# Optimization experiments

Measured on AMD Instinct MI355X. Metric: run time of the kernel, lower is better.

Reference implementation:

```python
import jax, jax.numpy as jnp
import numpy as np
import math

H = 8
D_MODEL = 512
D_K = D_MODEL // H          # 64, per-head value dim
D_QK = D_K // 2             # 32, per-head query/key dim
B, S = 2, 4096


def setup_inputs() -> dict:
    key = jax.random.key(0)
    ks = jax.random.split(key, 20)
    std = 0.02
    inp = {
        'query': jax.random.normal(ks[0], (B, S, D_MODEL), jnp.float32),
        'key':   jax.random.normal(ks[1], (B, S, D_MODEL), jnp.float32),
        'value': jax.random.normal(ks[2], (B, S, D_MODEL), jnp.float32),
        # MLP_q: d_model -> 2*d_model -> d_model/2
        'Wq1': jax.random.normal(ks[3], (D_MODEL, 2 * D_MODEL), jnp.float32) * std,
        'bq1': jnp.zeros((2 * D_MODEL,), jnp.float32),
        'Wq2': jax.random.normal(ks[4], (2 * D_MODEL, D_MODEL // 2), jnp.float32) * std,
        'bq2': jnp.zeros((D_MODEL // 2,), jnp.float32),
        # MLP_k: d_model -> 2*d_model -> d_model/2
        'Wk1': jax.random.normal(ks[5], (D_MODEL, 2 * D_MODEL), jnp.float32) * std,
        'bk1': jnp.zeros((2 * D_MODEL,), jnp.float32),
        'Wk2': jax.random.normal(ks[6], (2 * D_MODEL, D_MODEL // 2), jnp.float32) * std,
        'bk2': jnp.zeros((D_MODEL // 2,), jnp.float32),
        # linear_v and output linear: d_model -> d_model
        'Wv': jax.random.normal(ks[7], (D_MODEL, D_MODEL), jnp.float32) * std,
        'bv': jnp.zeros((D_MODEL,), jnp.float32),
        'Wo': jax.random.normal(ks[8], (D_MODEL, D_MODEL), jnp.float32) * std,
        'bo': jnp.zeros((D_MODEL,), jnp.float32),
    }
    return inp


def reference(query, key, value, Wq1, bq1, Wq2, bq2, Wk1, bk1, Wk2, bk2, Wv, bv, Wo, bo):
    nb = query.shape[0]
    # MLP_q / MLP_k: Linear -> exact GELU -> Linear (torch GELU default is erf)
    q = jax.nn.gelu(query @ Wq1 + bq1, approximate=False) @ Wq2 + bq2   # [B,S,D_MODEL/2]
    k = jax.nn.gelu(key   @ Wk1 + bk1, approximate=False) @ Wk2 + bk2   # [B,S,D_MODEL/2]
    v = value @ Wv + bv                                                  # [B,S,D_MODEL]

    q = q.reshape(nb, -1, H, D_QK)   # [B,S,H,d_qk]
    k = k.reshape(nb, -1, H, D_QK)
    v = v.reshape(nb, -1, H, D_K)    # [B,S,H,d_k]

    # scores scaled by sqrt(d_qk) since query.size(-1) == d_k//2 in the original
    scores = jnp.einsum('bqhd,bkhd->bhqk', q, k) / math.sqrt(D_QK)  # [B,H,S,S]
    p = jax.nn.softmax(scores, axis=-1)
    x = jnp.einsum('bhqk,bkhd->bqhd', p, v).reshape(nb, -1, H * D_K)  # [B,S,D_MODEL]
    return x @ Wo + bo
```

## Files before the change

### kernel.cpp

```cpp
#include <hip/hip_runtime.h>
#include <math.h>

typedef __attribute__((ext_vector_type(8))) short short8;
typedef __bf16 bf16x8 __attribute__((ext_vector_type(8)));
typedef __attribute__((ext_vector_type(4))) float f32x4;
typedef __attribute__((ext_vector_type(16))) float f32x16;

__device__ inline short f2bf(float f) {
    unsigned u = __builtin_bit_cast(unsigned, f);
    u += 0x7fff + ((u >> 16) & 1);
    return (short)(u >> 16);
}
__device__ inline float bf2f(short h) {
    return __builtin_bit_cast(float, ((unsigned)(unsigned short)h) << 16);
}
__device__ inline float gelu_f(float x) {
    return 0.5f * x * (1.f + erff(x * 0.70710678118654752f));
}

__global__ __launch_bounds__(256) void cast3(
    const float* __restrict__ q, const float* __restrict__ k,
    const float* __restrict__ v,
    short* __restrict__ qc, short* __restrict__ kc, short* __restrict__ vc)
{
    const float* src = blockIdx.y == 0 ? q : (blockIdx.y == 1 ? k : v);
    short* dst = blockIdx.y == 0 ? qc : (blockIdx.y == 1 ? kc : vc);
    size_t i = ((size_t)blockIdx.x * 256 + threadIdx.x) * 8;
    float4 a = *(const float4*)(src + i);
    float4 b = *(const float4*)(src + i + 4);
    short8 o;
    o[0] = f2bf(a.x); o[1] = f2bf(a.y); o[2] = f2bf(a.z); o[3] = f2bf(a.w);
    o[4] = f2bf(b.x); o[5] = f2bf(b.y); o[6] = f2bf(b.z); o[7] = f2bf(b.w);
    *(short8*)(void*)(dst + i) = o;
}

__global__ __launch_bounds__(256) void wprep(
    const float* __restrict__ Wq1, const float* __restrict__ Wk1,
    const float* __restrict__ Wq2, const float* __restrict__ Wk2,
    const float* __restrict__ Wv,  const float* __restrict__ Wo,
    short* __restrict__ Wq1t, short* __restrict__ Wk1t,
    short* __restrict__ Wq2t, short* __restrict__ Wk2t,
    short* __restrict__ Wvt,  short* __restrict__ Wo3t)
{
    int id = blockIdx.x;
    const float* W; short* Wt; int K, N; int t3 = 0;
    if (id < 512)       { W = Wq1; Wt = Wq1t; K = 512;  N = 1024; }
    else if (id < 1024) { W = Wk1; Wt = Wk1t; K = 512;  N = 1024; id -= 512; }
    else if (id < 1280) { W = Wq2; Wt = Wq2t; K = 1024; N = 256;  id -= 1024; }
    else if (id < 1536) { W = Wk2; Wt = Wk2t; K = 1024; N = 256;  id -= 1280; }
    else if (id < 1792) { W = Wv;  Wt = Wvt;  K = 512;  N = 512;  id -= 1536; }
    else                { W = Wo;  Wt = Wo3t; K = 512;  N = 512;  id -= 1792; t3 = 1; }
    int nx = N >> 5;
    int n0 = (id % nx) * 32, k0 = (id / nx) * 32;

    __shared__ float T[32][33];
    int tid = threadIdx.x;
    int r = tid >> 3, c4 = (tid & 7) * 4;
    float4 v = *(const float4*)&W[(size_t)(k0 + r) * N + n0 + c4];
    T[r][c4 + 0] = v.x; T[r][c4 + 1] = v.y; T[r][c4 + 2] = v.z; T[r][c4 + 3] = v.w;
    __syncthreads();
    if (!t3) {
        short4 o;
        o.x = f2bf(T[c4 + 0][r]);
        o.y = f2bf(T[c4 + 1][r]);
        o.z = f2bf(T[c4 + 2][r]);
        o.w = f2bf(T[c4 + 3][r]);
        *(short4*)&Wt[(size_t)(n0 + r) * K + k0 + c4] = o;
    } else {
        short4 hi, lo;
        float f;
        f = T[c4 + 0][r]; hi.x = f2bf(f); lo.x = f2bf(f - bf2f(hi.x));
        f = T[c4 + 1][r]; hi.y = f2bf(f); lo.y = f2bf(f - bf2f(hi.y));
        f = T[c4 + 2][r]; hi.z = f2bf(f); lo.z = f2bf(f - bf2f(hi.z));
        f = T[c4 + 3][r]; hi.w = f2bf(f); lo.w = f2bf(f - bf2f(hi.w));
        short* d = Wt + (size_t)(n0 + r) * 3 * K + k0 + c4;
        *(short4*)d = hi;
        *(short4*)(d + K) = lo;
        *(short4*)(d + 2 * K) = hi;
    }
}

template <int ACT, int OUTF32, int BN>
__global__ __launch_bounds__(256) void gemm_bt(
    const short* __restrict__ A0, const short* __restrict__ A1,
    const short* __restrict__ B0, const short* __restrict__ B1,
    const float* __restrict__ b0, const float* __restrict__ b1,
    void* C0_, void* C1_,
    float s0, float s1, int nbn, int N, int K)
{
    constexpr int NT = BN / 32;
    const int z = blockIdx.z;
    const short* A = z ? A1 : A0;
    const short* B = z ? B1 : B0;
    const float* bias = z ? b1 : b0;
    void* C_ = z ? C1_ : C0_;
    const float scale = z ? s1 : s0;

    const int L = blockIdx.x;
    const int xcd = L & 7;
    const int per = L >> 3;
    const int bn = (per % nbn) * BN;
    const int bm = ((per / nbn) * 8 + xcd) * 128;

    const int tid = threadIdx.x;
    const int w = tid >> 6;
    const int lane = tid & 63;
    const int l15 = lane & 15, quad = lane >> 4;
    const int wm = (w >> 1) * 64, wn = (w & 1) * (BN / 2);

    __shared__ __align__(16) short As[128 * 64];
    __shared__ __align__(16) short Bs[BN * 64];

    f32x4 acc[4][NT];
#pragma unroll
    for (int mt = 0; mt < 4; ++mt)
#pragma unroll
        for (int nt = 0; nt < NT; ++nt) acc[mt][nt] = (f32x4){0.f, 0.f, 0.f, 0.f};

    for (int k0 = 0; k0 < K; k0 += 64) {
#pragma unroll
        for (int i = 0; i < 4; ++i) {
            int ga = tid + i * 256;
            int row = ga >> 3, g = ga & 7;
            short8 aval = *(const short8*)(const void*)&A[(size_t)(bm + row) * K + k0 + g * 8];
            *(short8*)(void*)&As[row * 64 + ((g ^ (row & 7)) * 8)] = aval;
        }
#pragma unroll
        for (int i = 0; i < BN / 32; ++i) {
            int gb = tid + i * 256;
            int row = gb >> 3, g = gb & 7;
            short8 bval = *(const short8*)(const void*)&B[(size_t)(bn + row) * K + k0 + g * 8];
            *(short8*)(void*)&Bs[row * 64 + ((g ^ (row & 7)) * 8)] = bval;
        }
        __syncthreads();

#pragma unroll
        for (int ks = 0; ks < 2; ++ks) {
            bf16x8 af[4], bfr[NT];
#pragma unroll
            for (int t = 0; t < 4; ++t) {
                int row = wm + t * 16 + l15;
                af[t] = __builtin_bit_cast(bf16x8,
                    *(const short8*)(const void*)&As[row * 64 + (((ks * 4 + quad) ^ (row & 7)) * 8)]);
            }
#pragma unroll
            for (int t = 0; t < NT; ++t) {
                int row = wn + t * 16 + l15;
                bfr[t] = __builtin_bit_cast(bf16x8,
                    *(const short8*)(const void*)&Bs[row * 64 + (((ks * 4 + quad) ^ (row & 7)) * 8)]);
            }
#pragma unroll
            for (int mt = 0; mt < 4; ++mt)
#pragma unroll
                for (int nt = 0; nt < NT; ++nt)
                    acc[mt][nt] = __builtin_amdgcn_mfma_f32_16x16x32_bf16(af[mt], bfr[nt], acc[mt][nt], 0, 0, 0);
        }
        __syncthreads();
    }

    float bv[NT];
#pragma unroll
    for (int nt = 0; nt < NT; ++nt) bv[nt] = bias[bn + wn + nt * 16 + l15];
#pragma unroll
    for (int mt = 0; mt < 4; ++mt)
#pragma unroll
        for (int r = 0; r < 4; ++r) {
            int row = bm + wm + mt * 16 + quad * 4 + r;
#pragma unroll
            for (int nt = 0; nt < NT; ++nt) {
                float v = acc[mt][nt][r] + bv[nt];
                if (ACT) v = gelu_f(v);
                v *= scale;
                int col = bn + wn + nt * 16 + l15;
                if (OUTF32) ((float*)C_)[(size_t)row * N + col] = v;
                else        ((short*)C_)[(size_t)row * N + col] = f2bf(v);
            }
        }
}

__global__ __launch_bounds__(256) void repack_k(
    const short* __restrict__ kb, short* __restrict__ kfr)
{
    const int kt = blockIdx.x, bh = blockIdx.y;
    const int b = bh >> 3, h = bh & 7;
    const int t = threadIdx.x;
    const int c = t >> 6, l = t & 63;
    const int nt = c >> 1, ks = c & 1;
    int key = kt * 64 + nt * 32 + (l & 31);
    int k = ks * 16 + (l >> 5) * 8;
    short8 v = *(const short8*)(const void*)&kb[(size_t)(b * 4096 + key) * 256 + h * 32 + k];
    *(short8*)(void*)&kfr[((((size_t)bh * 64 + kt) * 4 + c) * 64 + l) * 8] = v;
}

__global__ __launch_bounds__(256) void repack_v(
    const short* __restrict__ vbb, short* __restrict__ vfr)
{
    const int kt = blockIdx.x, bh = blockIdx.y;
    const int b = bh >> 3, h = bh & 7;
    const int t = threadIdx.x;
    __shared__ short Vt[64][72];

#pragma unroll
    for (int it = 0; it < 2; ++it) {
        int idx = t + it * 256;
        int keyr = idx >> 3, c8 = (idx & 7) * 8;
        *(short8*)(void*)&Vt[keyr][c8] =
            *(const short8*)(const void*)&vbb[(size_t)(b * 4096 + kt * 64 + keyr) * 512 + h * 64 + c8];
    }
    __syncthreads();
#pragma unroll
    for (int it = 0; it < 2; ++it) {
        int chunk = (t >> 6) * 2 + it;
        int l = t & 63;
        int dt = chunk >> 2, ks = chunk & 3;
        short8 o;
#pragma unroll
        for (int j = 0; j < 8; ++j)
            o[j] = Vt[ks * 16 + (l >> 5) * 8 + j][dt * 32 + (l & 31)];
        *(short8*)(void*)&vfr[((((size_t)bh * 64 + kt) * 8 + chunk) * 64 + l) * 8] = o;
    }
}

__global__ __launch_bounds__(256) void flash_ks(
    const short* __restrict__ qb, const short* __restrict__ kfr,
    const short* __restrict__ vfr, short* __restrict__ xb3)
{
    const int L = blockIdx.x;
    const int xcd = L & 7;
    const int idx = L >> 3;
    const int bh = xcd * 2 + (idx & 1);
    const int qt = idx >> 1;
    const int b = bh >> 3, h = bh & 7;
    const int w = threadIdx.x >> 6;
    const int qg = w >> 1;
    const int kh = w & 1;
    const int lane = threadIdx.x & 63;
    const int l31 = lane & 31;
    const int half = lane >> 5;

    __shared__ __align__(16) char smem[18432];
    short* Pw = (short*)smem + w * 2304;

    const short* qrow = qb + (size_t)(b * 4096 + qt * 64 + qg * 32 + l31) * 256 + h * 32 + half * 8;
    bf16x8 qf0 = __builtin_bit_cast(bf16x8, *(const short8*)(const void*)qrow);
    bf16x8 qf1 = __builtin_bit_cast(bf16x8, *(const short8*)(const void*)(qrow + 16));

    f32x16 O0{}, O1{};
    float la = 0.f;

    const short* kbase = kfr + ((size_t)bh * 64) * 4 * 512 + lane * 8;
    const short* vbase = vfr + ((size_t)bh * 64) * 8 * 512 + lane * 8;

#pragma unroll 1
    for (int t = 0; t < 32; ++t) {
        const int kt = kh * 32 + t;
        bf16x8 kc[4], vc[8];
        const short* kp = kbase + (size_t)kt * 4 * 512;
        const short* vp = vbase + (size_t)kt * 8 * 512;
#pragma unroll
        for (int c = 0; c < 4; ++c)
            kc[c] = __builtin_bit_cast(bf16x8, *(const short8*)(const void*)(kp + c * 512));
#pragma unroll
        for (int c = 0; c < 8; ++c)
            vc[c] = __builtin_bit_cast(bf16x8, *(const short8*)(const void*)(vp + c * 512));

        f32x16 zero{};
        f32x16 s0 = __builtin_amdgcn_mfma_f32_32x32x16_bf16(kc[0], qf0, zero, 0, 0, 0);
        s0 = __builtin_amdgcn_mfma_f32_32x32x16_bf16(kc[1], qf1, s0, 0, 0, 0);
        f32x16 s1 = __builtin_amdgcn_mfma_f32_32x32x16_bf16(kc[2], qf0, zero, 0, 0, 0);
        s1 = __builtin_amdgcn_mfma_f32_32x32x16_bf16(kc[3], qf1, s1, 0, 0, 0);

#pragma unroll
        for (int nt = 0; nt < 2; ++nt) {
            const f32x16& s = nt ? s1 : s0;
#pragma unroll
            for (int r2 = 0; r2 < 4; ++r2) {
                float p0 = __builtin_amdgcn_exp2f(s[r2 * 4 + 0]);
                float p1 = __builtin_amdgcn_exp2f(s[r2 * 4 + 1]);
                float p2 = __builtin_amdgcn_exp2f(s[r2 * 4 + 2]);
                float p3 = __builtin_amdgcn_exp2f(s[r2 * 4 + 3]);
                unsigned pk01 = __builtin_amdgcn_perm(
                    __builtin_bit_cast(unsigned, p1), __builtin_bit_cast(unsigned, p0), 0x07060302u);
                unsigned pk23 = __builtin_amdgcn_perm(
                    __builtin_bit_cast(unsigned, p3), __builtin_bit_cast(unsigned, p2), 0x07060302u);
                la += __builtin_bit_cast(float, pk01 << 16)
                    + __builtin_bit_cast(float, pk01 & 0xffff0000u)
                    + __builtin_bit_cast(float, pk23 << 16)
                    + __builtin_bit_cast(float, pk23 & 0xffff0000u);
                int2 pk; pk.x = (int)pk01; pk.y = (int)pk23;
                *(int2*)(void*)&Pw[l31 * 72 + nt * 32 + r2 * 8 + half * 4] = pk;
            }
        }

        bf16x8 pf[4];
#pragma unroll
        for (int ks = 0; ks < 4; ++ks)
            pf[ks] = __builtin_bit_cast(bf16x8,
                *(const short8*)(const void*)&Pw[l31 * 72 + ks * 16 + half * 8]);
#pragma unroll
        for (int ks = 0; ks < 4; ++ks) {
            O0 = __builtin_amdgcn_mfma_f32_32x32x16_bf16(pf[ks], vc[ks], O0, 0, 0, 0);
            O1 = __builtin_amdgcn_mfma_f32_32x32x16_bf16(pf[ks], vc[4 + ks], O1, 0, 0, 0);
        }
    }

    la += __shfl_xor(la, 32);

    __syncthreads();
    float* redO = (float*)smem;
    float* redl = (float*)(smem + 16896);
    if (half == 0) redl[(qg * 2 + kh) * 32 + l31] = la;
    if (kh == 1) {
        float* Bo = redO + qg * 32 * 66;
#pragma unroll
        for (int r = 0; r < 16; ++r) {
            int q = (r & 3) + 8 * (r >> 2) + 4 * half;
            Bo[q * 66 + l31] = O0[r];
            Bo[q * 66 + 32 + l31] = O1[r];
        }
    }
    __syncthreads();
    if (kh == 0) {
        const float* Bo = redO + qg * 32 * 66;
#pragma unroll
        for (int r = 0; r < 16; ++r) {
            int q = (r & 3) + 8 * (r >> 2) + 4 * half;
            float o0 = O0[r] + Bo[q * 66 + l31];
            float o1 = O1[r] + Bo[q * 66 + 32 + l31];
            float inv = 1.f / (redl[qg * 64 + l31 ? 0 : 0], redl[(qg * 2 + 0) * 32 + q] + redl[(qg * 2 + 1) * 32 + q]);
            float x0 = o0 * inv, x1 = o1 * inv;
            short hi0 = f2bf(x0), hi1 = f2bf(x1);
            short lo0 = f2bf(x0 - bf2f(hi0)), lo1 = f2bf(x1 - bf2f(hi1));
            size_t row = (size_t)(b * 4096 + qt * 64 + qg * 32 + q);
            short* d = xb3 + row * 1536 + h * 64 + l31;
            d[0] = hi0;    d[32] = hi1;
            d[512] = hi0;  d[544] = hi1;
            d[1024] = lo0; d[1056] = lo1;
        }
    }
}

extern "C" void kernel_launch(void* const* d_in, const int* in_sizes, int n_in,
                              void* d_out, int out_size, void* d_ws, size_t ws_size,
                              hipStream_t stream)
{
    const float* query = (const float*)d_in[0];
    const float* key   = (const float*)d_in[1];
    const float* value = (const float*)d_in[2];
    const float* Wq1   = (const float*)d_in[3];
    const float* bq1   = (const float*)d_in[4];
    const float* Wq2   = (const float*)d_in[5];
    const float* bq2   = (const float*)d_in[6];
    const float* Wk1   = (const float*)d_in[7];
    const float* bk1   = (const float*)d_in[8];
    const float* Wk2   = (const float*)d_in[9];
    const float* bk2   = (const float*)d_in[10];
    const float* Wv    = (const float*)d_in[11];
    const float* bv    = (const float*)d_in[12];
    const float* Wo    = (const float*)d_in[13];
    const float* bo    = (const float*)d_in[14];
    float* out = (float*)d_out;

    char* ws = (char*)d_ws;
    short* H1q   = (short*)(ws + 0);
    short* H1k   = (short*)(ws + 16777216);
    short* xb3   = (short*)(ws + 0);
    short* qcast = (short*)(ws + 33554432);
    short* kcast = (short*)(ws + 41943040);
    short* vcast = (short*)(ws + 50331648);
    short* qbb   = (short*)(ws + 33554432);
    short* kbb   = (short*)(ws + 37748736);
    short* vbb   = (short*)(ws + 41943040);
    short* kfr   = (short*)(ws + 50331648);
    short* vfr   = (short*)(ws + 54525952);
    short* Wq1t  = (short*)(ws + 62914560);
    short* Wk1t  = (short*)(ws + 63963136);
    short* Wq2t  = (short*)(ws + 65011712);
    short* Wk2t  = (short*)(ws + 65536000);
    short* Wvt   = (short*)(ws + 66060288);
    short* Wo3t  = (short*)(ws + 66584576);

    dim3 blk(256);
    const float qscale = 0.17677669529663687f * 1.4426950408889634f;

    cast3<<<dim3(2048, 3), blk, 0, stream>>>(query, key, value, qcast, kcast, vcast);
    wprep<<<dim3(2048), blk, 0, stream>>>(Wq1, Wk1, Wq2, Wk2, Wv, Wo,
                                          Wq1t, Wk1t, Wq2t, Wk2t, Wvt, Wo3t);

    gemm_bt<1, 0, 128><<<dim3(8 * 64, 1, 2), blk, 0, stream>>>(
        qcast, kcast, Wq1t, Wk1t, bq1, bk1, H1q, H1k, 1.f, 1.f, 8, 1024, 512);
    gemm_bt<0, 0, 64><<<dim3(4 * 64, 1, 2), blk, 0, stream>>>(
        H1q, H1k, Wq2t, Wk2t, bq2, bk2, qbb, kbb, qscale, 1.f, 4, 256, 1024);
    gemm_bt<0, 0, 64><<<dim3(8 * 64, 1, 1), blk, 0, stream>>>(
        vcast, vcast, Wvt, Wvt, bv, bv, vbb, vbb, 1.f, 1.f, 8, 512, 512);
    repack_k<<<dim3(64, 16), blk, 0, stream>>>(kbb, kfr);
    repack_v<<<dim3(64, 16), blk, 0, stream>>>(vbb, vfr);
    flash_ks<<<dim3(1024), dim3(256), 0, stream>>>(qbb, kfr, vfr, xb3);
    gemm_bt<0, 1, 64><<<dim3(8 * 64, 1, 1), blk, 0, stream>>>(
        xb3, xb3, Wo3t, Wo3t, bo, bo, out, out, 1.f, 1.f, 8, 512, 1536);
}
```

Baseline: 307.1 us.

## Drop split-bf16 output projection, compute softmax denominator via MFMA, merge prep kernels

```diff
diff --git a/kernel.cpp b/kernel.cpp
--- a/kernel.cpp
+++ b/kernel.cpp
@@ -18,66 +18,54 @@
     return 0.5f * x * (1.f + erff(x * 0.70710678118654752f));
 }
 
-__global__ __launch_bounds__(256) void cast3(
+__global__ __launch_bounds__(256) void prep_all(
     const float* __restrict__ q, const float* __restrict__ k,
     const float* __restrict__ v,
-    short* __restrict__ qc, short* __restrict__ kc, short* __restrict__ vc)
-{
-    const float* src = blockIdx.y == 0 ? q : (blockIdx.y == 1 ? k : v);
-    short* dst = blockIdx.y == 0 ? qc : (blockIdx.y == 1 ? kc : vc);
-    size_t i = ((size_t)blockIdx.x * 256 + threadIdx.x) * 8;
-    float4 a = *(const float4*)(src + i);
-    float4 b = *(const float4*)(src + i + 4);
-    short8 o;
-    o[0] = f2bf(a.x); o[1] = f2bf(a.y); o[2] = f2bf(a.z); o[3] = f2bf(a.w);
-    o[4] = f2bf(b.x); o[5] = f2bf(b.y); o[6] = f2bf(b.z); o[7] = f2bf(b.w);
-    *(short8*)(void*)(dst + i) = o;
-}
-
-__global__ __launch_bounds__(256) void wprep(
+    short* __restrict__ qc, short* __restrict__ kc, short* __restrict__ vc,
     const float* __restrict__ Wq1, const float* __restrict__ Wk1,
     const float* __restrict__ Wq2, const float* __restrict__ Wk2,
     const float* __restrict__ Wv,  const float* __restrict__ Wo,
     short* __restrict__ Wq1t, short* __restrict__ Wk1t,
     short* __restrict__ Wq2t, short* __restrict__ Wk2t,
-    short* __restrict__ Wvt,  short* __restrict__ Wo3t)
+    short* __restrict__ Wvt,  short* __restrict__ Wot)
 {
     int id = blockIdx.x;
-    const float* W; short* Wt; int K, N; int t3 = 0;
+    if (id < 6144) {
+        const float* src = id < 2048 ? q : (id < 4096 ? k : v);
+        short* dst = id < 2048 ? qc : (id < 4096 ? kc : vc);
+        int blk = id & 2047;
+        size_t i = ((size_t)blk * 256 + threadIdx.x) * 8;
+        float4 a = *(const float4*)(src + i);
+        float4 b = *(const float4*)(src + i + 4);
+        short8 o;
+        o[0] = f2bf(a.x); o[1] = f2bf(a.y); o[2] = f2bf(a.z); o[3] = f2bf(a.w);
+        o[4] = f2bf(b.x); o[5] = f2bf(b.y); o[6] = f2bf(b.z); o[7] = f2bf(b.w);
+        *(short8*)(void*)(dst + i) = o;
+        return;
+    }
+    id -= 6144;
+    const float* W; short* Wt; int K, N;
     if (id < 512)       { W = Wq1; Wt = Wq1t; K = 512;  N = 1024; }
     else if (id < 1024) { W = Wk1; Wt = Wk1t; K = 512;  N = 1024; id -= 512; }
     else if (id < 1280) { W = Wq2; Wt = Wq2t; K = 1024; N = 256;  id -= 1024; }
     else if (id < 1536) { W = Wk2; Wt = Wk2t; K = 1024; N = 256;  id -= 1280; }
     else if (id < 1792) { W = Wv;  Wt = Wvt;  K = 512;  N = 512;  id -= 1536; }
-    else                { W = Wo;  Wt = Wo3t; K = 512;  N = 512;  id -= 1792; t3 = 1; }
+    else                { W = Wo;  Wt = Wot;  K = 512;  N = 512;  id -= 1792; }
     int nx = N >> 5;
     int n0 = (id % nx) * 32, k0 = (id / nx) * 32;
 
     __shared__ float T[32][33];
     int tid = threadIdx.x;
     int r = tid >> 3, c4 = (tid & 7) * 4;
-    float4 v = *(const float4*)&W[(size_t)(k0 + r) * N + n0 + c4];
-    T[r][c4 + 0] = v.x; T[r][c4 + 1] = v.y; T[r][c4 + 2] = v.z; T[r][c4 + 3] = v.w;
+    float4 v4 = *(const float4*)&W[(size_t)(k0 + r) * N + n0 + c4];
+    T[r][c4 + 0] = v4.x; T[r][c4 + 1] = v4.y; T[r][c4 + 2] = v4.z; T[r][c4 + 3] = v4.w;
     __syncthreads();
-    if (!t3) {
-        short4 o;
-        o.x = f2bf(T[c4 + 0][r]);
-        o.y = f2bf(T[c4 + 1][r]);
-        o.z = f2bf(T[c4 + 2][r]);
-        o.w = f2bf(T[c4 + 3][r]);
-        *(short4*)&Wt[(size_t)(n0 + r) * K + k0 + c4] = o;
-    } else {
-        short4 hi, lo;
-        float f;
-        f = T[c4 + 0][r]; hi.x = f2bf(f); lo.x = f2bf(f - bf2f(hi.x));
-        f = T[c4 + 1][r]; hi.y = f2bf(f); lo.y = f2bf(f - bf2f(hi.y));
-        f = T[c4 + 2][r]; hi.z = f2bf(f); lo.z = f2bf(f - bf2f(hi.z));
-        f = T[c4 + 3][r]; hi.w = f2bf(f); lo.w = f2bf(f - bf2f(hi.w));
-        short* d = Wt + (size_t)(n0 + r) * 3 * K + k0 + c4;
-        *(short4*)d = hi;
-        *(short4*)(d + K) = lo;
-        *(short4*)(d + 2 * K) = hi;
-    }
+    short4 o;
+    o.x = f2bf(T[c4 + 0][r]);
+    o.y = f2bf(T[c4 + 1][r]);
+    o.z = f2bf(T[c4 + 2][r]);
+    o.w = f2bf(T[c4 + 3][r]);
+    *(short4*)&Wt[(size_t)(n0 + r) * K + k0 + c4] = o;
 }
 
 template <int ACT, int OUTF32, int BN>
@@ -223,7 +211,7 @@
 
 __global__ __launch_bounds__(256) void flash_ks(
     const short* __restrict__ qb, const short* __restrict__ kfr,
-    const short* __restrict__ vfr, short* __restrict__ xb3)
+    const short* __restrict__ vfr, short* __restrict__ xbb)
 {
     const int L = blockIdx.x;
     const int xcd = L & 7;
@@ -245,8 +233,12 @@
     bf16x8 qf0 = __builtin_bit_cast(bf16x8, *(const short8*)(const void*)qrow);
     bf16x8 qf1 = __builtin_bit_cast(bf16x8, *(const short8*)(const void*)(qrow + 16));
 
-    f32x16 O0{}, O1{};
-    float la = 0.f;
+    short8 ones_s;
+#pragma unroll
+    for (int j = 0; j < 8; ++j) ones_s[j] = (short)0x3F80;
+    const bf16x8 onesf = __builtin_bit_cast(bf16x8, ones_s);
+
+    f32x16 O0{}, O1{}, lacc{};
 
     const short* kbase = kfr + ((size_t)bh * 64) * 4 * 512 + lane * 8;
     const short* vbase = vfr + ((size_t)bh * 64) * 8 * 512 + lane * 8;
@@ -283,10 +275,6 @@
                     __builtin_bit_cast(unsigned, p1), __builtin_bit_cast(unsigned, p0), 0x07060302u);
                 unsigned pk23 = __builtin_amdgcn_perm(
                     __builtin_bit_cast(unsigned, p3), __builtin_bit_cast(unsigned, p2), 0x07060302u);
-                la += __builtin_bit_cast(float, pk01 << 16)
-                    + __builtin_bit_cast(float, pk01 & 0xffff0000u)
-                    + __builtin_bit_cast(float, pk23 << 16)
-                    + __builtin_bit_cast(float, pk23 & 0xffff0000u);
                 int2 pk; pk.x = (int)pk01; pk.y = (int)pk23;
                 *(int2*)(void*)&Pw[l31 * 72 + nt * 32 + r2 * 8 + half * 4] = pk;
             }
@@ -301,15 +289,20 @@
         for (int ks = 0; ks < 4; ++ks) {
             O0 = __builtin_amdgcn_mfma_f32_32x32x16_bf16(pf[ks], vc[ks], O0, 0, 0, 0);
             O1 = __builtin_amdgcn_mfma_f32_32x32x16_bf16(pf[ks], vc[4 + ks], O1, 0, 0, 0);
-        }
-    }
-
-    la += __shfl_xor(la, 32);
+            lacc = __builtin_amdgcn_mfma_f32_32x32x16_bf16(pf[ks], onesf, lacc, 0, 0, 0);
+        }
+    }
 
     __syncthreads();
     float* redO = (float*)smem;
     float* redl = (float*)(smem + 16896);
-    if (half == 0) redl[(qg * 2 + kh) * 32 + l31] = la;
+    if (l31 == 0) {
+#pragma unroll
+        for (int r = 0; r < 16; ++r) {
+            int q = (r & 3) + 8 * (r >> 2) + 4 * half;
+            redl[(qg * 2 + kh) * 32 + q] = lacc[r];
+        }
+    }
     if (kh == 1) {
         float* Bo = redO + qg * 32 * 66;
 #pragma unroll
@@ -327,15 +320,11 @@
             int q = (r & 3) + 8 * (r >> 2) + 4 * half;
             float o0 = O0[r] + Bo[q * 66 + l31];
             float o1 = O1[r] + Bo[q * 66 + 32 + l31];
-            float inv = 1.f / (redl[qg * 64 + l31 ? 0 : 0], redl[(qg * 2 + 0) * 32 + q] + redl[(qg * 2 + 1) * 32 + q]);
-            float x0 = o0 * inv, x1 = o1 * inv;
-            short hi0 = f2bf(x0), hi1 = f2bf(x1);
-            short lo0 = f2bf(x0 - bf2f(hi0)), lo1 = f2bf(x1 - bf2f(hi1));
+            float inv = 1.f / (redl[(qg * 2 + 0) * 32 + q] + redl[(qg * 2 + 1) * 32 + q]);
             size_t row = (size_t)(b * 4096 + qt * 64 + qg * 32 + q);
-            short* d = xb3 + row * 1536 + h * 64 + l31;
-            d[0] = hi0;    d[32] = hi1;
-            d[512] = hi0;  d[544] = hi1;
-            d[1024] = lo0; d[1056] = lo1;
+            short* d = xbb + row * 512 + h * 64 + l31;
+            d[0] = f2bf(o0 * inv);
+            d[32] = f2bf(o1 * inv);
         }
     }
 }
@@ -364,7 +353,7 @@
     char* ws = (char*)d_ws;
     short* H1q   = (short*)(ws + 0);
     short* H1k   = (short*)(ws + 16777216);
-    short* xb3   = (short*)(ws + 0);
+    short* xbb   = (short*)(ws + 0);
     short* qcast = (short*)(ws + 33554432);
     short* kcast = (short*)(ws + 41943040);
     short* vcast = (short*)(ws + 50331648);
@@ -378,14 +367,14 @@
     short* Wq2t  = (short*)(ws + 65011712);
     short* Wk2t  = (short*)(ws + 65536000);
     short* Wvt   = (short*)(ws + 66060288);
-    short* Wo3t  = (short*)(ws + 66584576);
+    short* Wot   = (short*)(ws + 66584576);
 
     dim3 blk(256);
     const float qscale = 0.17677669529663687f * 1.4426950408889634f;
 
-    cast3<<<dim3(2048, 3), blk, 0, stream>>>(query, key, value, qcast, kcast, vcast);
-    wprep<<<dim3(2048), blk, 0, stream>>>(Wq1, Wk1, Wq2, Wk2, Wv, Wo,
-                                          Wq1t, Wk1t, Wq2t, Wk2t, Wvt, Wo3t);
+    prep_all<<<dim3(8192), blk, 0, stream>>>(
+        query, key, value, qcast, kcast, vcast,
+        Wq1, Wk1, Wq2, Wk2, Wv, Wo, Wq1t, Wk1t, Wq2t, Wk2t, Wvt, Wot);
 
     gemm_bt<1, 0, 128><<<dim3(8 * 64, 1, 2), blk, 0, stream>>>(
         qcast, kcast, Wq1t, Wk1t, bq1, bk1, H1q, H1k, 1.f, 1.f, 8, 1024, 512);
@@ -395,7 +384,7 @@
         vcast, vcast, Wvt, Wvt, bv, bv, vbb, vbb, 1.f, 1.f, 8, 512, 512);
     repack_k<<<dim3(64, 16), blk, 0, stream>>>(kbb, kfr);
     repack_v<<<dim3(64, 16), blk, 0, stream>>>(vbb, vfr);
-    flash_ks<<<dim3(1024), dim3(256), 0, stream>>>(qbb, kfr, vfr, xb3);
+    flash_ks<<<dim3(1024), blk, 0, stream>>>(qbb, kfr, vfr, xbb);
     gemm_bt<0, 1, 64><<<dim3(8 * 64, 1, 1), blk, 0, stream>>>(
-        xb3, xb3, Wo3t, Wo3t, bo, bo, out, out, 1.f, 1.f, 8, 512, 1536);
-}
+        xbb, xbb, Wot, Wot, bo, bo, out, out, 1.f, 1.f, 8, 512, 512);
+}
```

After: 280.9 us. -8.5%, faster.
